# Performance work log

Measured on AMD Instinct MI355X. Metric: run time of the kernel, lower is better.

Reference implementation:

```python
import jax, jax.numpy as jnp
import numpy as np

N = 50000      # nodes (B-rep faces)
E = 800000     # directed edges (avg degree 16)
F_IN = 9       # 8 surface-type flags + is_feature
H1, H2, C = 512, 128, 2


def setup_inputs() -> dict:
    key = jax.random.key(0)
    ks = jax.random.split(key, 8)
    x = jax.random.normal(ks[0], (N, F_IN), dtype=jnp.float32)
    edge_index = jax.random.randint(ks[1], (2, E), 0, N, dtype=jnp.int64)
    W1 = jax.random.normal(ks[2], (F_IN, H1), dtype=jnp.float32) / np.sqrt(F_IN)
    b1 = jnp.zeros((H1,), dtype=jnp.float32)
    W2 = jax.random.normal(ks[3], (H1, H2), dtype=jnp.float32) / np.sqrt(H1)
    b2 = jnp.zeros((H2,), dtype=jnp.float32)
    W3 = jax.random.normal(ks[4], (H2, C), dtype=jnp.float32) / np.sqrt(H2)
    b3 = jnp.zeros((C,), dtype=jnp.float32)
    return {"x": x, "W1": W1, "b1": b1, "W2": W2, "b2": b2,
            "W3": W3, "b3": b3, "edge_index": edge_index}


def reference(x, W1, b1, W2, b2, W3, b3, edge_index):
    n = x.shape[0]
    self_idx = jnp.arange(n, dtype=edge_index.dtype)
    # GCN with self-loops and symmetric normalization (PyG gcn_norm)
    src = jnp.concatenate([edge_index[0], self_idx])  # [E+N]
    dst = jnp.concatenate([edge_index[1], self_idx])  # [E+N]
    deg = jax.ops.segment_sum(jnp.ones_like(src, dtype=x.dtype), dst, num_segments=n)
    dinv = jnp.where(deg > 0, jax.lax.rsqrt(jnp.maximum(deg, 1.0)), 0.0)
    norm = dinv[src] * dinv[dst]  # [E+N]

    def gcn(h, W, b):
        h = h @ W                                   # [N, out]
        msg = h[src] * norm[:, None]                # gather + scale
        return jax.ops.segment_sum(msg, dst, num_segments=n) + b  # scatter-add

    h = jax.nn.relu(gcn(x, W1, b1))
    h = jax.nn.relu(gcn(h, W2, b2))
    # F.dropout with training=False is identity (inference mode)
    h = gcn(h, W3, b3)
    return jax.nn.log_softmax(h, axis=1)
```

## Files before the change

### kernel.cpp

```cpp
#include <hip/hip_runtime.h>
#include <hip/hip_bf16.h>

typedef __attribute__((ext_vector_type(8))) short short8;
typedef __attribute__((ext_vector_type(4))) float float4v;
typedef unsigned int uint;

#define NBLK 192

static __device__ __forceinline__ float2 up_bf2(uint v) {
    float2 r;
    r.x = __uint_as_float(v << 16);
    r.y = __uint_as_float(v & 0xffff0000u);
    return r;
}
static __device__ __forceinline__ short f2bf_bits(float x) {
    union { __hip_bfloat16 h; short s; } u;
    u.h = __float2bfloat16(x);
    return u.s;
}


__global__ __launch_bounds__(256) void k_hist(const int* __restrict__ dst, int E, int chunk,
        int shift, int nbuck, int* __restrict__ histBlk) {
    __shared__ int h[256];
    h[threadIdx.x] = 0;
    __syncthreads();
    int blk = blockIdx.x;
    int e0 = blk * chunk, e1 = min(E, e0 + chunk);
    for (int e = e0 + threadIdx.x; e < e1; e += 256)
        atomicAdd(&h[dst[e] >> shift], 1);
    __syncthreads();
    if (threadIdx.x < nbuck) histBlk[threadIdx.x * NBLK + blk] = h[threadIdx.x];
}


__global__ __launch_bounds__(256) void k_btot(const int* __restrict__ histBlk,
                                              int* __restrict__ btot) {
    __shared__ int s[256];
    int b = blockIdx.x, t = threadIdx.x;
    s[t] = (t < NBLK) ? histBlk[b * NBLK + t] : 0;
    __syncthreads();
    for (int off = 128; off; off >>= 1) {
        if (t < off) s[t] += s[t + off];
        __syncthreads();
    }
    if (t == 0) btot[b] = s[0];
}


__global__ __launch_bounds__(256) void k_bscan(const int* __restrict__ histBlk,
        const int* __restrict__ btot, int nbuck,
        int* __restrict__ baseBlk, int* __restrict__ bucketBase) {
    __shared__ int s[256], sb[256];
    int b = blockIdx.x, t = threadIdx.x;
    int v = (t < NBLK) ? histBlk[b * NBLK + t] : 0;
    s[t] = v;
    sb[t] = (t < nbuck) ? btot[t] : 0;
    __syncthreads();
    for (int off = 1; off < 256; off <<= 1) {
        int u = (t >= off) ? s[t - off] : 0;
        int u2 = (t >= off) ? sb[t - off] : 0;
        __syncthreads();
        s[t] += u;
        sb[t] += u2;
        __syncthreads();
    }
    int base = (b > 0) ? sb[b - 1] : 0;
    if (t < NBLK) baseBlk[b * NBLK + t] = base + s[t] - v;
    if (t == 0) bucketBase[b] = base;
}


__global__ __launch_bounds__(256) void k_scatterbin(const int* __restrict__ src,
        const int* __restrict__ dst, int E, int chunk, int shift, int nbuck,
        const int* __restrict__ baseBlk, uint* __restrict__ binned) {
    __shared__ int cur[256];
    int blk = blockIdx.x;
    if (threadIdx.x < nbuck) cur[threadIdx.x] = baseBlk[threadIdx.x * NBLK + blk];
    __syncthreads();
    int e0 = blk * chunk, e1 = min(E, e0 + chunk);
    int mask = (1 << shift) - 1;
    for (int e = e0 + threadIdx.x; e < e1; e += 256) {
        int d = dst[e];
        int pos = atomicAdd(&cur[d >> shift], 1);
        binned[pos] = (uint)src[e] | ((uint)(d & mask) << 24);
    }
}


__global__ __launch_bounds__(256) void k_csrbuild(const uint* __restrict__ binned,
        const int* __restrict__ bucketBase, const float* __restrict__ x,
        int E, int shift, int n, int nbuck,
        int* __restrict__ row_ptr, float* __restrict__ dinv, float* __restrict__ xs,
        int* __restrict__ csr) {
    __shared__ int cnt[256], lcur[256];
    int b = blockIdx.x, t = threadIdx.x;
    cnt[t] = 0;
    __syncthreads();
    int lo = bucketBase[b];
    int hi = (b + 1 < nbuck) ? bucketBase[b + 1] : E;
    for (int e = lo + t; e < hi; e += 256)
        atomicAdd(&cnt[binned[e] >> 24], 1);
    __syncthreads();
    int c = cnt[t];
    lcur[t] = c;
    __syncthreads();
    for (int off = 1; off < 256; off <<= 1) {
        int u = (t >= off) ? lcur[t - off] : 0;
        __syncthreads();
        lcur[t] += u;
        __syncthreads();
    }
    int node0 = b << shift;
    int nodeEnd = min(n, (b + 1) << shift);
    int cntNodes = nodeEnd - node0;
    int myBase = lo + lcur[t] - c;
    if (t < cntNodes) {
        row_ptr[node0 + t] = myBase;
        dinv[node0 + t] = rsqrtf((float)(c + 1));
    }
    if (b == nbuck - 1 && t == 0) row_ptr[n] = E;
    for (int j = t; j < cntNodes * 9; j += 256) {
        int nl = j / 9, f = j - nl * 9;
        float dnl = rsqrtf((float)(cnt[nl] + 1));
        xs[(size_t)(node0 + nl) * 9 + f] = dnl * x[(size_t)(node0 + nl) * 9 + f];
    }
    __syncthreads();
    lcur[t] = myBase;
    __syncthreads();
    for (int e = lo + t; e < hi; e += 256) {
        uint p = binned[e];
        int pos = atomicAdd(&lcur[p >> 24], 1);
        csr[pos] = (int)(p & 0xFFFFFF);
    }
}


__global__ __launch_bounds__(256) void k_agg1(const float* __restrict__ xs,
                       const float* __restrict__ dinv,
                       const int* __restrict__ row_ptr, const int* __restrict__ csr,
                       __hip_bfloat16* __restrict__ aggx_bf, int n) {
    int node = blockIdx.x * 16 + (threadIdx.x >> 4);
    if (node >= n) return;
    int f = threadIdx.x & 15;
    bool act = f < 9;
    float acc = act ? xs[node * 9 + f] : 0.f;
    int e0 = row_ptr[node], e1 = row_ptr[node + 1];
    int e = e0;
    for (; e + 4 <= e1; e += 4) {
        int s0 = csr[e], s1 = csr[e + 1], s2 = csr[e + 2], s3 = csr[e + 3];
        float x0 = act ? xs[s0 * 9 + f] : 0.f;
        float x1 = act ? xs[s1 * 9 + f] : 0.f;
        float x2 = act ? xs[s2 * 9 + f] : 0.f;
        float x3 = act ? xs[s3 * 9 + f] : 0.f;
        acc += (x0 + x1) + (x2 + x3);
    }
    for (; e < e1; ++e) {
        int sA = csr[e];
        acc += act ? xs[sA * 9 + f] : 0.f;
    }
    float v = act ? dinv[node] * acc : 0.f;
    __hip_bfloat16* op = aggx_bf + (size_t)node * 32;
    union { __hip_bfloat16 h; short s; } u;
    u.h = __float2bfloat16(v);
    reinterpret_cast<short*>(op)[f] = u.s;
    reinterpret_cast<short*>(op)[16 + f] = 0;
}


__global__ __launch_bounds__(256) void k_w1frag(const float* __restrict__ W1,
                                                __hip_bfloat16* __restrict__ W1frag) {
    int t = blockIdx.x * 256 + threadIdx.x;
    if (t >= 32 * 64) return;
    int ctile = t >> 6, lane = t & 63;
    int col = ctile * 16 + (lane & 15);
    int k0 = (lane >> 4) * 8;
    short8 o;
#pragma unroll
    for (int j = 0; j < 8; ++j) {
        int k = k0 + j;
        o[j] = f2bf_bits(k < 9 ? W1[k * 512 + col] : 0.f);
    }
    *reinterpret_cast<short8*>(W1frag + (size_t)t * 8) = o;
}

__global__ __launch_bounds__(512, 2) void k_l12(const __hip_bfloat16* __restrict__ aggx_bf,
                       const __hip_bfloat16* __restrict__ W1frag, const float* __restrict__ b1,
                       const float* __restrict__ W2, const float* __restrict__ dinv,
                       __hip_bfloat16* __restrict__ t2, int n, int npair) {
    __shared__ short bsh[64 * 128 * 8];
    __shared__ short h1s[8][2][16][40];
    int t = threadIdx.x;

    for (int idx = t; idx < 64 * 128; idx += 512) {
        int kb = idx >> 7, c = idx & 127;
        const float* wp = W2 + (size_t)(kb * 8) * 128 + c;
        short8 o;
#pragma unroll
        for (int j = 0; j < 8; ++j) o[j] = f2bf_bits(wp[j * 128]);
        *reinterpret_cast<short8*>(bsh + (size_t)idx * 8) = o;
    }
    __syncthreads();

    int wid = t >> 6, lane = t & 63;
    int pair = blockIdx.x * 8 + wid;
    if (pair >= npair) return;
    int r = lane & 15, quad = lane >> 4;
    short (*hs0)[40] = h1s[wid][0];
    short (*hs1)[40] = h1s[wid][1];

    int m0 = pair << 5;
    short8 aagg0 = *reinterpret_cast<const short8*>(
        aggx_bf + (size_t)(m0 + r) * 32 + quad * 8);
    short8 aagg1 = *reinterpret_cast<const short8*>(
        aggx_bf + (size_t)(m0 + 16 + r) * 32 + quad * 8);

    float4v acc0[8], acc1[8];
#pragma unroll
    for (int cg = 0; cg < 8; ++cg) {
        acc0[cg] = (float4v){0, 0, 0, 0};
        acc1[cg] = (float4v){0, 0, 0, 0};
    }

    for (int kt = 0; kt < 16; ++kt) {
        short8 bf0 = *reinterpret_cast<const short8*>(
            W1frag + ((size_t)(2 * kt) * 64 + lane) * 8);
        short8 bf1 = *reinterpret_cast<const short8*>(
            W1frag + ((size_t)(2 * kt + 1) * 64 + lane) * 8);
        float4v c00 = __builtin_amdgcn_mfma_f32_16x16x32_bf16(
            aagg0, bf0, (float4v){0, 0, 0, 0}, 0, 0, 0);
        float4v c01 = __builtin_amdgcn_mfma_f32_16x16x32_bf16(
            aagg0, bf1, (float4v){0, 0, 0, 0}, 0, 0, 0);
        float4v c10 = __builtin_amdgcn_mfma_f32_16x16x32_bf16(
            aagg1, bf0, (float4v){0, 0, 0, 0}, 0, 0, 0);
        float4v c11 = __builtin_amdgcn_mfma_f32_16x16x32_bf16(
            aagg1, bf1, (float4v){0, 0, 0, 0}, 0, 0, 0);
        float bb0 = b1[kt * 32 + r];
        float bb1 = b1[kt * 32 + 16 + r];
#pragma unroll
        for (int i = 0; i < 4; ++i) {
            int row = quad * 4 + i;
            hs0[row][r]      = f2bf_bits(fmaxf(c00[i] + bb0, 0.f));
            hs0[row][16 + r] = f2bf_bits(fmaxf(c01[i] + bb1, 0.f));
            hs1[row][r]      = f2bf_bits(fmaxf(c10[i] + bb0, 0.f));
            hs1[row][16 + r] = f2bf_bits(fmaxf(c11[i] + bb1, 0.f));
        }
        short8 am0 = *reinterpret_cast<const short8*>(&hs0[r][quad * 8]);
        short8 am1 = *reinterpret_cast<const short8*>(&hs1[r][quad * 8]);
#pragma unroll
        for (int cg = 0; cg < 8; ++cg) {
            short8 b = *reinterpret_cast<const short8*>(
                bsh + (size_t)(((kt * 4 + quad) * 128) + cg * 16 + r) * 8);
            acc0[cg] = __builtin_amdgcn_mfma_f32_16x16x32_bf16(am0, b, acc0[cg], 0, 0, 0);
            acc1[cg] = __builtin_amdgcn_mfma_f32_16x16x32_bf16(am1, b, acc1[cg], 0, 0, 0);
        }
    }

#pragma unroll
    for (int i = 0; i < 4; ++i) {
        int node0 = m0 + quad * 4 + i;
        if (node0 < n) {
            float di = dinv[node0];
            __hip_bfloat16* op = t2 + (size_t)node0 * 128 + r;
#pragma unroll
            for (int cg = 0; cg < 8; ++cg)
                op[cg * 16] = __float2bfloat16(di * acc0[cg][i]);
        }
        int node1 = m0 + 16 + quad * 4 + i;
        if (node1 < n) {
            float di = dinv[node1];
            __hip_bfloat16* op = t2 + (size_t)node1 * 128 + r;
#pragma unroll
            for (int cg = 0; cg < 8; ++cg)
                op[cg * 16] = __float2bfloat16(di * acc1[cg][i]);
        }
    }
}


__global__ __launch_bounds__(256) void k_agg2(const uint* __restrict__ t2u,
                       const float* __restrict__ dinv,
                       const int* __restrict__ row_ptr, const int* __restrict__ csr,
                       const float* __restrict__ b2, const float* __restrict__ W3,
                       float2* __restrict__ t3, int n) {
    int node = blockIdx.x * 4 + (threadIdx.x >> 6);
    if (node >= n) return;
    int lane = threadIdx.x & 63;
    int half = lane >> 5;
    int cl = lane & 31;
    const uint2* t2v = reinterpret_cast<const uint2*>(t2u);

    float a0 = 0.f, a1 = 0.f, a2 = 0.f, a3 = 0.f;
    if (half == 0) {
        uint2 sv = t2v[(size_t)node * 32 + cl];
        float2 pa = up_bf2(sv.x), pb = up_bf2(sv.y);
        a0 = pa.x; a1 = pa.y; a2 = pb.x; a3 = pb.y;
    }

    int e0 = row_ptr[node], e1 = row_ptr[node + 1];
    int eb = e0;
    for (; eb + 16 <= e1; eb += 16) {
        int si[8];
        uint2 ri[8];
#pragma unroll
        for (int j = 0; j < 8; ++j) si[j] = csr[eb + half + 2 * j];
#pragma unroll
        for (int j = 0; j < 8; ++j) ri[j] = t2v[(size_t)si[j] * 32 + cl];
#pragma unroll
        for (int j = 0; j < 8; ++j) {
            float2 qa = up_bf2(ri[j].x), qb = up_bf2(ri[j].y);
            a0 += qa.x; a1 += qa.y; a2 += qb.x; a3 += qb.y;
        }
    }
    for (; eb + 4 <= e1; eb += 4) {
        int s0 = csr[eb + half], s1 = csr[eb + half + 2];
        uint2 r0 = t2v[(size_t)s0 * 32 + cl];
        uint2 r1 = t2v[(size_t)s1 * 32 + cl];
        float2 qa = up_bf2(r0.x), qb = up_bf2(r0.y);
        float2 qc = up_bf2(r1.x), qd = up_bf2(r1.y);
        a0 += qa.x + qc.x; a1 += qa.y + qc.y;
        a2 += qb.x + qd.x; a3 += qb.y + qd.y;
    }
    for (int e = eb + half; e < e1; e += 2) {
        uint2 rv = t2v[(size_t)csr[e] * 32 + cl];
        float2 qa = up_bf2(rv.x), qb = up_bf2(rv.y);
        a0 += qa.x; a1 += qa.y; a2 += qb.x; a3 += qb.y;
    }

    a0 += __shfl_xor(a0, 32);
    a1 += __shfl_xor(a1, 32);
    a2 += __shfl_xor(a2, 32);
    a3 += __shfl_xor(a3, 32);

    float di = dinv[node];
    float4 bb = *reinterpret_cast<const float4*>(b2 + 4 * cl);
    float h0 = fmaxf(di * a0 + bb.x, 0.f);
    float h1v = fmaxf(di * a1 + bb.y, 0.f);
    float h2 = fmaxf(di * a2 + bb.z, 0.f);
    float h3 = fmaxf(di * a3 + bb.w, 0.f);
    float4 wlo = *reinterpret_cast<const float4*>(W3 + 8 * cl);
    float4 whi = *reinterpret_cast<const float4*>(W3 + 8 * cl + 4);
    float c0 = h0 * wlo.x + h1v * wlo.z + h2 * whi.x + h3 * whi.z;
    float c1 = h0 * wlo.y + h1v * wlo.w + h2 * whi.y + h3 * whi.w;
#pragma unroll
    for (int off = 16; off; off >>= 1) {
        c0 += __shfl_xor(c0, off);
        c1 += __shfl_xor(c1, off);
    }
    if (lane == 0) t3[node] = make_float2(di * c0, di * c1);
}


__global__ void k_agg3(const float2* __restrict__ t3, const float* __restrict__ dinv,
                       const int* __restrict__ row_ptr, const int* __restrict__ csr,
                       const float* __restrict__ b3, float2* __restrict__ outv, int n) {
    int node = blockIdx.x * blockDim.x + threadIdx.x;
    if (node >= n) return;
    float2 s = t3[node];
    float a0 = s.x, a1 = s.y;
    int e0 = row_ptr[node], e1 = row_ptr[node + 1];
    int e = e0;
    for (; e + 4 <= e1; e += 4) {
        int s0 = csr[e], s1 = csr[e + 1], s2 = csr[e + 2], s3 = csr[e + 3];
        float2 q0 = t3[s0], q1 = t3[s1], q2 = t3[s2], q3 = t3[s3];
        a0 += q0.x + q1.x + q2.x + q3.x;
        a1 += q0.y + q1.y + q2.y + q3.y;
    }
    for (; e < e1; ++e) {
        float2 q0 = t3[csr[e]];
        a0 += q0.x;
        a1 += q0.y;
    }
    float di = dinv[node];
    float z0 = di * a0 + b3[0];
    float z1 = di * a1 + b3[1];
    float m = fmaxf(z0, z1);
    float lse = m + logf(expf(z0 - m) + expf(z1 - m));
    outv[node] = make_float2(z0 - lse, z1 - lse);
}


extern "C" void kernel_launch(void* const* d_in, const int* in_sizes, int n_in,
                              void* d_out, int out_size, void* d_ws, size_t ws_size,
                              hipStream_t stream) {
    const float* x  = (const float*)d_in[0];
    const float* W1 = (const float*)d_in[1];
    const float* b1 = (const float*)d_in[2];
    const float* W2 = (const float*)d_in[3];
    const float* b2 = (const float*)d_in[4];
    const float* W3 = (const float*)d_in[5];
    const float* b3 = (const float*)d_in[6];
    const int* edges = (const int*)d_in[7];

    int n = in_sizes[0] / 9;
    int E = in_sizes[7] / 2;
    const int* src = edges;
    const int* dst = edges + E;

    char* p = (char*)d_ws;
    auto alloc = [&](size_t bytes) {
        char* q = p;
        p += (bytes + 511) & ~(size_t)511;
        return q;
    };
    float* dinv       = (float*)alloc((size_t)n * 4);
    int*   row_ptr    = (int*)alloc((size_t)(n + 1) * 4);
    int*   csr        = (int*)alloc((size_t)E * 4);
    int*   histBlk    = (int*)alloc((size_t)256 * NBLK * 4);
    int*   baseBlk    = (int*)alloc((size_t)256 * NBLK * 4);
    int*   btot       = (int*)alloc(256 * 4);
    int*   bucketBase = (int*)alloc(256 * 4);
    uint*  binned     = (uint*)alloc((size_t)E * 4);
    float* xs         = (float*)alloc((size_t)n * 9 * 4);
    __hip_bfloat16* aggx_bf = (__hip_bfloat16*)alloc((size_t)(n + 64) * 32 * 2);
    __hip_bfloat16* W1frag  = (__hip_bfloat16*)alloc((size_t)32 * 64 * 8 * 2);
    __hip_bfloat16* t2 = (__hip_bfloat16*)alloc((size_t)n * 128 * 2);
    float2* t3 = (float2*)alloc((size_t)n * 8);

    const int B = 256;
    int shift = 8;
    int nbuck = ((n - 1) >> shift) + 1;
    int chunk = (E + NBLK - 1) / NBLK;

    k_hist<<<NBLK, B, 0, stream>>>(dst, E, chunk, shift, nbuck, histBlk);
    k_btot<<<nbuck, B, 0, stream>>>(histBlk, btot);
    k_bscan<<<nbuck, B, 0, stream>>>(histBlk, btot, nbuck, baseBlk, bucketBase);
    k_scatterbin<<<NBLK, B, 0, stream>>>(src, dst, E, chunk, shift, nbuck, baseBlk, binned);
    k_csrbuild<<<nbuck, B, 0, stream>>>(binned, bucketBase, x, E, shift, n, nbuck,
                                        row_ptr, dinv, xs, csr);

    k_w1frag<<<8, B, 0, stream>>>(W1, W1frag);
    k_agg1<<<(n + 15) / 16, B, 0, stream>>>(xs, dinv, row_ptr, csr, aggx_bf, n);

    int ntile = (n + 15) / 16;
    int npair = (ntile + 1) / 2;
    k_l12<<<(npair + 7) / 8, 512, 0, stream>>>(aggx_bf, W1frag, b1, W2, dinv, t2, n, npair);
    k_agg2<<<(n + 3) / 4, 256, 0, stream>>>((const uint*)t2, dinv, row_ptr, csr, b2, W3, t3, n);

    k_agg3<<<(n + B - 1) / B, B, 0, stream>>>(t3, dinv, row_ptr, csr, b3, (float2*)d_out, n);
}
```

Measured before the change: 194.1 us.

## Fuse CSR build stages into one kernel with grid barriers; merge W1 fragment prep

Replaces the five CSR-construction kernels (histogram, bucket totals, bucket scan, scatter-bin, CSR build) with a single persistent kernel that separates the phases with atomic-counter grid barriers. The W1 fragment conversion is folded into the first aggregation kernel as extra blocks. The goal is to remove several kernel launch gaps. The cost is spin-wait barriers that rely on all 196 blocks being co-resident, plus a memset to reset the barrier counters on every call.

```diff
diff --git a/kernel.cpp b/kernel.cpp
--- a/kernel.cpp
+++ b/kernel.cpp
@@ -5,7 +5,7 @@
 typedef __attribute__((ext_vector_type(4))) float float4v;
 typedef unsigned int uint;
 
-#define NBLK 192
+#define NBLK 196
 
 static __device__ __forceinline__ float2 up_bf2(uint v) {
     float2 r;
@@ -19,128 +19,154 @@
     return u.s;
 }
 
-
-__global__ __launch_bounds__(256) void k_hist(const int* __restrict__ dst, int E, int chunk,
-        int shift, int nbuck, int* __restrict__ histBlk) {
-    __shared__ int h[256];
-    h[threadIdx.x] = 0;
+static __device__ __forceinline__ void gbar(int* c, int idx, int nb) {
     __syncthreads();
-    int blk = blockIdx.x;
-    int e0 = blk * chunk, e1 = min(E, e0 + chunk);
-    for (int e = e0 + threadIdx.x; e < e1; e += 256)
-        atomicAdd(&h[dst[e] >> shift], 1);
+    if (threadIdx.x == 0) {
+        __threadfence();
+        atomicAdd(&c[idx], 1);
+        while (atomicAdd(&c[idx], 0) < nb)
+            __builtin_amdgcn_s_sleep(2);
+        __threadfence();
+    }
     __syncthreads();
-    if (threadIdx.x < nbuck) histBlk[threadIdx.x * NBLK + blk] = h[threadIdx.x];
-}
-
-
-__global__ __launch_bounds__(256) void k_btot(const int* __restrict__ histBlk,
-                                              int* __restrict__ btot) {
-    __shared__ int s[256];
-    int b = blockIdx.x, t = threadIdx.x;
-    s[t] = (t < NBLK) ? histBlk[b * NBLK + t] : 0;
+}
+
+
+__global__ __launch_bounds__(256) void k_prep(const int* __restrict__ src,
+        const int* __restrict__ dst, const float* __restrict__ x,
+        int E, int n, int shift, int nbuck, int nblk,
+        int* __restrict__ histBlk, int* __restrict__ btot,
+        int* __restrict__ baseBlk, int* __restrict__ bucketBase,
+        uint* __restrict__ binned, int* __restrict__ row_ptr,
+        float* __restrict__ dinv, float* __restrict__ xs,
+        int* __restrict__ csr, int* __restrict__ bar) {
+    __shared__ int sh[256], sh2[256];
+    int blk = blockIdx.x, t = threadIdx.x;
+    int nb = gridDim.x;
+    int chunk = (E + nblk - 1) / nblk;
+
+    sh[t] = 0;
     __syncthreads();
-    for (int off = 128; off; off >>= 1) {
-        if (t < off) s[t] += s[t + off];
-        __syncthreads();
-    }
-    if (t == 0) btot[b] = s[0];
-}
-
-
-__global__ __launch_bounds__(256) void k_bscan(const int* __restrict__ histBlk,
-        const int* __restrict__ btot, int nbuck,
-        int* __restrict__ baseBlk, int* __restrict__ bucketBase) {
-    __shared__ int s[256], sb[256];
-    int b = blockIdx.x, t = threadIdx.x;
-    int v = (t < NBLK) ? histBlk[b * NBLK + t] : 0;
-    s[t] = v;
-    sb[t] = (t < nbuck) ? btot[t] : 0;
-    __syncthreads();
-    for (int off = 1; off < 256; off <<= 1) {
-        int u = (t >= off) ? s[t - off] : 0;
-        int u2 = (t >= off) ? sb[t - off] : 0;
-        __syncthreads();
-        s[t] += u;
-        sb[t] += u2;
-        __syncthreads();
-    }
-    int base = (b > 0) ? sb[b - 1] : 0;
-    if (t < NBLK) baseBlk[b * NBLK + t] = base + s[t] - v;
-    if (t == 0) bucketBase[b] = base;
-}
-
-
-__global__ __launch_bounds__(256) void k_scatterbin(const int* __restrict__ src,
-        const int* __restrict__ dst, int E, int chunk, int shift, int nbuck,
-        const int* __restrict__ baseBlk, uint* __restrict__ binned) {
-    __shared__ int cur[256];
-    int blk = blockIdx.x;
-    if (threadIdx.x < nbuck) cur[threadIdx.x] = baseBlk[threadIdx.x * NBLK + blk];
-    __syncthreads();
-    int e0 = blk * chunk, e1 = min(E, e0 + chunk);
-    int mask = (1 << shift) - 1;
-    for (int e = e0 + threadIdx.x; e < e1; e += 256) {
-        int d = dst[e];
-        int pos = atomicAdd(&cur[d >> shift], 1);
-        binned[pos] = (uint)src[e] | ((uint)(d & mask) << 24);
-    }
-}
-
-
-__global__ __launch_bounds__(256) void k_csrbuild(const uint* __restrict__ binned,
-        const int* __restrict__ bucketBase, const float* __restrict__ x,
-        int E, int shift, int n, int nbuck,
-        int* __restrict__ row_ptr, float* __restrict__ dinv, float* __restrict__ xs,
-        int* __restrict__ csr) {
-    __shared__ int cnt[256], lcur[256];
-    int b = blockIdx.x, t = threadIdx.x;
-    cnt[t] = 0;
-    __syncthreads();
-    int lo = bucketBase[b];
-    int hi = (b + 1 < nbuck) ? bucketBase[b + 1] : E;
-    for (int e = lo + t; e < hi; e += 256)
-        atomicAdd(&cnt[binned[e] >> 24], 1);
-    __syncthreads();
-    int c = cnt[t];
-    lcur[t] = c;
-    __syncthreads();
-    for (int off = 1; off < 256; off <<= 1) {
-        int u = (t >= off) ? lcur[t - off] : 0;
-        __syncthreads();
-        lcur[t] += u;
-        __syncthreads();
-    }
-    int node0 = b << shift;
-    int nodeEnd = min(n, (b + 1) << shift);
-    int cntNodes = nodeEnd - node0;
-    int myBase = lo + lcur[t] - c;
-    if (t < cntNodes) {
-        row_ptr[node0 + t] = myBase;
-        dinv[node0 + t] = rsqrtf((float)(c + 1));
-    }
-    if (b == nbuck - 1 && t == 0) row_ptr[n] = E;
-    for (int j = t; j < cntNodes * 9; j += 256) {
-        int nl = j / 9, f = j - nl * 9;
-        float dnl = rsqrtf((float)(cnt[nl] + 1));
-        xs[(size_t)(node0 + nl) * 9 + f] = dnl * x[(size_t)(node0 + nl) * 9 + f];
-    }
-    __syncthreads();
-    lcur[t] = myBase;
-    __syncthreads();
-    for (int e = lo + t; e < hi; e += 256) {
-        uint p = binned[e];
-        int pos = atomicAdd(&lcur[p >> 24], 1);
-        csr[pos] = (int)(p & 0xFFFFFF);
-    }
-}
-
-
-__global__ __launch_bounds__(256) void k_agg1(const float* __restrict__ xs,
+    if (blk < nblk) {
+        int e0 = blk * chunk, e1 = min(E, e0 + chunk);
+        for (int e = e0 + t; e < e1; e += 256)
+            atomicAdd(&sh[dst[e] >> shift], 1);
+        __syncthreads();
+        if (t < nbuck) histBlk[t * nblk + blk] = sh[t];
+    }
+    gbar(bar, 0, nb);
+
+    if (blk < nbuck) {
+        sh[t] = (t < nblk) ? histBlk[blk * nblk + t] : 0;
+        __syncthreads();
+        for (int off = 128; off; off >>= 1) {
+            if (t < off) sh[t] += sh[t + off];
+            __syncthreads();
+        }
+        if (t == 0) btot[blk] = sh[0];
+    }
+    gbar(bar, 1, nb);
+
+    if (blk < nbuck) {
+        int v = (t < nblk) ? histBlk[blk * nblk + t] : 0;
+        sh[t] = v;
+        sh2[t] = (t < nbuck) ? btot[t] : 0;
+        __syncthreads();
+        for (int off = 1; off < 256; off <<= 1) {
+            int u = (t >= off) ? sh[t - off] : 0;
+            int u2 = (t >= off) ? sh2[t - off] : 0;
+            __syncthreads();
+            sh[t] += u;
+            sh2[t] += u2;
+            __syncthreads();
+        }
+        int base = (blk > 0) ? sh2[blk - 1] : 0;
+        if (t < nblk) baseBlk[blk * nblk + t] = base + sh[t] - v;
+        if (t == 0) bucketBase[blk] = base;
+    }
+    gbar(bar, 2, nb);
+
+    if (blk < nblk) {
+        if (t < nbuck) sh[t] = baseBlk[t * nblk + blk];
+        __syncthreads();
+        int e0 = blk * chunk, e1 = min(E, e0 + chunk);
+        int mask = (1 << shift) - 1;
+        for (int e = e0 + t; e < e1; e += 256) {
+            int d = dst[e];
+            int pos = atomicAdd(&sh[d >> shift], 1);
+            binned[pos] = (uint)src[e] | ((uint)(d & mask) << 24);
+        }
+    }
+    gbar(bar, 3, nb);
+
+    if (blk < nbuck) {
+        int b = blk;
+        sh[t] = 0;
+        __syncthreads();
+        int lo = bucketBase[b];
+        int hi = (b + 1 < nbuck) ? bucketBase[b + 1] : E;
+        for (int e = lo + t; e < hi; e += 256)
+            atomicAdd(&sh[binned[e] >> 24], 1);
+        __syncthreads();
+        int c = sh[t];
+        sh2[t] = c;
+        __syncthreads();
+        for (int off = 1; off < 256; off <<= 1) {
+            int u = (t >= off) ? sh2[t - off] : 0;
+            __syncthreads();
+            sh2[t] += u;
+            __syncthreads();
+        }
+        int node0 = b << shift;
+        int nodeEnd = min(n, (b + 1) << shift);
+        int cntNodes = nodeEnd - node0;
+        int myBase = lo + sh2[t] - c;
+        if (t < cntNodes) {
+            row_ptr[node0 + t] = myBase;
+            dinv[node0 + t] = rsqrtf((float)(c + 1));
+        }
+        if (b == nbuck - 1 && t == 0) row_ptr[n] = E;
+        for (int j = t; j < cntNodes * 9; j += 256) {
+            int nl = j / 9, f = j - nl * 9;
+            float dnl = rsqrtf((float)(sh[nl] + 1));
+            xs[(size_t)(node0 + nl) * 9 + f] = dnl * x[(size_t)(node0 + nl) * 9 + f];
+        }
+        __syncthreads();
+        sh2[t] = myBase;
+        __syncthreads();
+        for (int e = lo + t; e < hi; e += 256) {
+            uint p = binned[e];
+            int pos = atomicAdd(&sh2[p >> 24], 1);
+            csr[pos] = (int)(p & 0xFFFFFF);
+        }
+    }
+}
+
+
+__global__ __launch_bounds__(256) void k_agg1w(const float* __restrict__ xs,
                        const float* __restrict__ dinv,
                        const int* __restrict__ row_ptr, const int* __restrict__ csr,
-                       __hip_bfloat16* __restrict__ aggx_bf, int n) {
-    int node = blockIdx.x * 16 + (threadIdx.x >> 4);
+                       const float* __restrict__ W1,
+                       __hip_bfloat16* __restrict__ aggx_bf,
+                       __hip_bfloat16* __restrict__ W1frag, int n, int nagg) {
+    int bid = blockIdx.x;
+    if (bid >= nagg) {
+        int t = (bid - nagg) * 256 + threadIdx.x;
+        if (t < 32 * 64) {
+            int ctile = t >> 6, lane = t & 63;
+            int col = ctile * 16 + (lane & 15);
+            int k0 = (lane >> 4) * 8;
+            short8 o;
+#pragma unroll
+            for (int j = 0; j < 8; ++j) {
+                int k = k0 + j;
+                o[j] = f2bf_bits(k < 9 ? W1[k * 512 + col] : 0.f);
+            }
+            *reinterpret_cast<short8*>(W1frag + (size_t)t * 8) = o;
+        }
+        return;
+    }
+    int node = bid * 16 + (threadIdx.x >> 4);
     if (node >= n) return;
     int f = threadIdx.x & 15;
     bool act = f < 9;
@@ -165,23 +191,6 @@
     u.h = __float2bfloat16(v);
     reinterpret_cast<short*>(op)[f] = u.s;
     reinterpret_cast<short*>(op)[16 + f] = 0;
-}
-
-
-__global__ __launch_bounds__(256) void k_w1frag(const float* __restrict__ W1,
-                                                __hip_bfloat16* __restrict__ W1frag) {
-    int t = blockIdx.x * 256 + threadIdx.x;
-    if (t >= 32 * 64) return;
-    int ctile = t >> 6, lane = t & 63;
-    int col = ctile * 16 + (lane & 15);
-    int k0 = (lane >> 4) * 8;
-    short8 o;
-#pragma unroll
-    for (int j = 0; j < 8; ++j) {
-        int k = k0 + j;
-        o[j] = f2bf_bits(k < 9 ? W1[k * 512 + col] : 0.f);
-    }
-    *reinterpret_cast<short8*>(W1frag + (size_t)t * 8) = o;
 }
 
 __global__ __launch_bounds__(512, 2) void k_l12(const __hip_bfloat16* __restrict__ aggx_bf,
@@ -410,6 +419,7 @@
     int*   baseBlk    = (int*)alloc((size_t)256 * NBLK * 4);
     int*   btot       = (int*)alloc(256 * 4);
     int*   bucketBase = (int*)alloc(256 * 4);
+    int*   bar        = (int*)alloc(64);
     uint*  binned     = (uint*)alloc((size_t)E * 4);
     float* xs         = (float*)alloc((size_t)n * 9 * 4);
     __hip_bfloat16* aggx_bf = (__hip_bfloat16*)alloc((size_t)(n + 64) * 32 * 2);
@@ -420,17 +430,16 @@
     const int B = 256;
     int shift = 8;
     int nbuck = ((n - 1) >> shift) + 1;
-    int chunk = (E + NBLK - 1) / NBLK;
-
-    k_hist<<<NBLK, B, 0, stream>>>(dst, E, chunk, shift, nbuck, histBlk);
-    k_btot<<<nbuck, B, 0, stream>>>(histBlk, btot);
-    k_bscan<<<nbuck, B, 0, stream>>>(histBlk, btot, nbuck, baseBlk, bucketBase);
-    k_scatterbin<<<NBLK, B, 0, stream>>>(src, dst, E, chunk, shift, nbuck, baseBlk, binned);
-    k_csrbuild<<<nbuck, B, 0, stream>>>(binned, bucketBase, x, E, shift, n, nbuck,
-                                        row_ptr, dinv, xs, csr);
-
-    k_w1frag<<<8, B, 0, stream>>>(W1, W1frag);
-    k_agg1<<<(n + 15) / 16, B, 0, stream>>>(xs, dinv, row_ptr, csr, aggx_bf, n);
+    int gridp = (nbuck > NBLK) ? nbuck : NBLK;
+
+    hipMemsetAsync(bar, 0, 16, stream);
+    k_prep<<<gridp, B, 0, stream>>>(src, dst, x, E, n, shift, nbuck, NBLK,
+                                    histBlk, btot, baseBlk, bucketBase,
+                                    binned, row_ptr, dinv, xs, csr, bar);
+
+    int nagg = (n + 15) / 16;
+    k_agg1w<<<nagg + 8, B, 0, stream>>>(xs, dinv, row_ptr, csr, W1,
+                                        aggx_bf, W1frag, n, nagg);
 
     int ntile = (n + 15) / 16;
     int npair = (ntile + 1) / 2;
```

Result: slower. 248.2 us (+27.8%).

## Precompute W2 bf16 fragments once and load MFMA B operands from global

Applied to the files above, without the earlier changes.

The W1 fragment conversion is merged into the agg1 kernel as extra blocks, and that kernel now also converts W2 to a bf16 fragment layout in global memory. k_l12 therefore no longer fills 128KB of shared memory from fp32 W2 in every block. It loads the B fragments for each k-step straight from global memory, which should be L2-resident. This removes a per-block prologue and a barrier, cuts LDS use (which may raise occupancy), and saves one launch, at the cost of more global/L2 loads inside the inner loop.

```diff
diff --git a/kernel.cpp b/kernel.cpp
--- a/kernel.cpp
+++ b/kernel.cpp
@@ -136,11 +136,44 @@
 }
 
 
-__global__ __launch_bounds__(256) void k_agg1(const float* __restrict__ xs,
+__global__ __launch_bounds__(256) void k_agg1w(const float* __restrict__ xs,
                        const float* __restrict__ dinv,
                        const int* __restrict__ row_ptr, const int* __restrict__ csr,
-                       __hip_bfloat16* __restrict__ aggx_bf, int n) {
-    int node = blockIdx.x * 16 + (threadIdx.x >> 4);
+                       const float* __restrict__ W1, const float* __restrict__ W2,
+                       __hip_bfloat16* __restrict__ aggx_bf,
+                       __hip_bfloat16* __restrict__ W1frag,
+                       __hip_bfloat16* __restrict__ W2frag, int n, int nagg) {
+    int bid = blockIdx.x;
+    if (bid >= nagg) {
+        int xb = bid - nagg;
+        if (xb < 8) {
+            int t = xb * 256 + threadIdx.x;
+            if (t < 32 * 64) {
+                int ctile = t >> 6, lane = t & 63;
+                int col = ctile * 16 + (lane & 15);
+                int k0 = (lane >> 4) * 8;
+                short8 o;
+#pragma unroll
+                for (int j = 0; j < 8; ++j) {
+                    int k = k0 + j;
+                    o[j] = f2bf_bits(k < 9 ? W1[k * 512 + col] : 0.f);
+                }
+                *reinterpret_cast<short8*>(W1frag + (size_t)t * 8) = o;
+            }
+        } else {
+            int t = (xb - 8) * 256 + threadIdx.x;
+            if (t < 64 * 128) {
+                int kb = t >> 7, c = t & 127;
+                const float* wp = W2 + (size_t)(kb * 8) * 128 + c;
+                short8 o;
+#pragma unroll
+                for (int j = 0; j < 8; ++j) o[j] = f2bf_bits(wp[j * 128]);
+                *reinterpret_cast<short8*>(W2frag + (size_t)t * 8) = o;
+            }
+        }
+        return;
+    }
+    int node = bid * 16 + (threadIdx.x >> 4);
     if (node >= n) return;
     int f = threadIdx.x & 15;
     bool act = f < 9;
@@ -167,41 +200,14 @@
     reinterpret_cast<short*>(op)[16 + f] = 0;
 }
 
-
-__global__ __launch_bounds__(256) void k_w1frag(const float* __restrict__ W1,
-                                                __hip_bfloat16* __restrict__ W1frag) {
-    int t = blockIdx.x * 256 + threadIdx.x;
-    if (t >= 32 * 64) return;
-    int ctile = t >> 6, lane = t & 63;
-    int col = ctile * 16 + (lane & 15);
-    int k0 = (lane >> 4) * 8;
-    short8 o;
-#pragma unroll
-    for (int j = 0; j < 8; ++j) {
-        int k = k0 + j;
-        o[j] = f2bf_bits(k < 9 ? W1[k * 512 + col] : 0.f);
-    }
-    *reinterpret_cast<short8*>(W1frag + (size_t)t * 8) = o;
-}
-
 __global__ __launch_bounds__(512, 2) void k_l12(const __hip_bfloat16* __restrict__ aggx_bf,
-                       const __hip_bfloat16* __restrict__ W1frag, const float* __restrict__ b1,
-                       const float* __restrict__ W2, const float* __restrict__ dinv,
+                       const __hip_bfloat16* __restrict__ W1frag,
+                       const __hip_bfloat16* __restrict__ W2frag,
+                       const float* __restrict__ b1,
+                       const float* __restrict__ dinv,
                        __hip_bfloat16* __restrict__ t2, int n, int npair) {
-    __shared__ short bsh[64 * 128 * 8];
     __shared__ short h1s[8][2][16][40];
     int t = threadIdx.x;
-
-    for (int idx = t; idx < 64 * 128; idx += 512) {
-        int kb = idx >> 7, c = idx & 127;
-        const float* wp = W2 + (size_t)(kb * 8) * 128 + c;
-        short8 o;
-#pragma unroll
-        for (int j = 0; j < 8; ++j) o[j] = f2bf_bits(wp[j * 128]);
-        *reinterpret_cast<short8*>(bsh + (size_t)idx * 8) = o;
-    }
-    __syncthreads();
-
     int wid = t >> 6, lane = t & 63;
     int pair = blockIdx.x * 8 + wid;
     if (pair >= npair) return;
@@ -237,6 +243,11 @@
             aagg1, bf1, (float4v){0, 0, 0, 0}, 0, 0, 0);
         float bb0 = b1[kt * 32 + r];
         float bb1 = b1[kt * 32 + 16 + r];
+        short8 bfr[8];
+#pragma unroll
+        for (int cg = 0; cg < 8; ++cg)
+            bfr[cg] = *reinterpret_cast<const short8*>(
+                W2frag + (size_t)(((kt * 4 + quad) * 128) + cg * 16 + r) * 8);
 #pragma unroll
         for (int i = 0; i < 4; ++i) {
             int row = quad * 4 + i;
@@ -249,10 +260,8 @@
         short8 am1 = *reinterpret_cast<const short8*>(&hs1[r][quad * 8]);
 #pragma unroll
         for (int cg = 0; cg < 8; ++cg) {
-            short8 b = *reinterpret_cast<const short8*>(
-                bsh + (size_t)(((kt * 4 + quad) * 128) + cg * 16 + r) * 8);
-            acc0[cg] = __builtin_amdgcn_mfma_f32_16x16x32_bf16(am0, b, acc0[cg], 0, 0, 0);
-            acc1[cg] = __builtin_amdgcn_mfma_f32_16x16x32_bf16(am1, b, acc1[cg], 0, 0, 0);
+            acc0[cg] = __builtin_amdgcn_mfma_f32_16x16x32_bf16(am0, bfr[cg], acc0[cg], 0, 0, 0);
+            acc1[cg] = __builtin_amdgcn_mfma_f32_16x16x32_bf16(am1, bfr[cg], acc1[cg], 0, 0, 0);
         }
     }
 
@@ -414,6 +423,7 @@
     float* xs         = (float*)alloc((size_t)n * 9 * 4);
     __hip_bfloat16* aggx_bf = (__hip_bfloat16*)alloc((size_t)(n + 64) * 32 * 2);
     __hip_bfloat16* W1frag  = (__hip_bfloat16*)alloc((size_t)32 * 64 * 8 * 2);
+    __hip_bfloat16* W2frag  = (__hip_bfloat16*)alloc((size_t)64 * 128 * 8 * 2);
     __hip_bfloat16* t2 = (__hip_bfloat16*)alloc((size_t)n * 128 * 2);
     float2* t3 = (float2*)alloc((size_t)n * 8);
 
@@ -429,12 +439,13 @@
     k_csrbuild<<<nbuck, B, 0, stream>>>(binned, bucketBase, x, E, shift, n, nbuck,
                                         row_ptr, dinv, xs, csr);
 
-    k_w1frag<<<8, B, 0, stream>>>(W1, W1frag);
-    k_agg1<<<(n + 15) / 16, B, 0, stream>>>(xs, dinv, row_ptr, csr, aggx_bf, n);
+    int nagg = (n + 15) / 16;
+    k_agg1w<<<nagg + 40, B, 0, stream>>>(xs, dinv, row_ptr, csr, W1, W2,
+                                         aggx_bf, W1frag, W2frag, n, nagg);
 
     int ntile = (n + 15) / 16;
     int npair = (ntile + 1) / 2;
-    k_l12<<<(npair + 7) / 8, 512, 0, stream>>>(aggx_bf, W1frag, b1, W2, dinv, t2, n, npair);
+    k_l12<<<(npair + 7) / 8, 512, 0, stream>>>(aggx_bf, W1frag, W2frag, b1, dinv, t2, n, npair);
     k_agg2<<<(n + 3) / 4, 256, 0, stream>>>((const uint*)t2, dinv, row_ptr, csr, b2, W3, t3, n);
 
     k_agg3<<<(n + B - 1) / B, B, 0, stream>>>(t3, dinv, row_ptr, csr, b3, (float2*)d_out, n);
```

New measurement: 196.3 us. No clear change (+1.1%).
